# Optimization experiments

Measured on AMD Instinct MI355X. Metric: run time of the kernel, lower is better.

The kernel has to match this reference:

```python
import jax, jax.numpy as jnp
import numpy as np

D_MODEL = 1024
NUM_HEADS = 16
HEAD_DIM = D_MODEL // NUM_HEADS


def setup_inputs() -> dict:
    key = jax.random.key(0)
    k_x, k_wq, k_wo = jax.random.split(key, 3)
    x = jax.random.normal(k_x, (2, 2048, D_MODEL), dtype=jnp.float32)
    # Xavier-uniform init to mirror _reset_parameters
    lim_qkv = float(np.sqrt(6.0 / (D_MODEL + 3 * D_MODEL)))
    lim_o = float(np.sqrt(6.0 / (D_MODEL + D_MODEL)))
    w_qkv = jax.random.uniform(k_wq, (3 * D_MODEL, D_MODEL), jnp.float32, -lim_qkv, lim_qkv)
    b_qkv = jnp.zeros((3 * D_MODEL,), jnp.float32)
    w_o = jax.random.uniform(k_wo, (D_MODEL, D_MODEL), jnp.float32, -lim_o, lim_o)
    b_o = jnp.zeros((D_MODEL,), jnp.float32)
    return {"x": x, "w_qkv": w_qkv, "b_qkv": b_qkv, "w_o": w_o, "b_o": b_o}


def reference(x, w_qkv, b_qkv, w_o, b_o):
    B, T, C = x.shape
    H, Dh = NUM_HEADS, HEAD_DIM
    # Fused QKV projection: [B,T,3C]
    qkv = jnp.einsum('btc,oc->bto', x, w_qkv) + b_qkv
    qkv = qkv.reshape(B, T, 3, H, Dh)
    q = qkv[:, :, 0].transpose(0, 2, 1, 3)  # [B,H,T,Dh]
    k = qkv[:, :, 1].transpose(0, 2, 1, 3)
    v = qkv[:, :, 2].transpose(0, 2, 1, 3)
    scale = 1.0 / jnp.sqrt(jnp.asarray(Dh, x.dtype))
    scores = jnp.einsum('bhqd,bhkd->bhqk', q, k) * scale  # [B,H,T,T]
    attn = jax.nn.softmax(scores, axis=-1)
    out = jnp.einsum('bhqk,bhkd->bhqd', attn, v)  # [B,H,T,Dh]
    out = out.transpose(0, 2, 1, 3).reshape(B, T, C)
    return jnp.einsum('btc,oc->bto', out, w_o) + b_o
```

## Files before the change

### kernel.cpp

```cpp
#include <hip/hip_runtime.h>
#include <math.h>

#define SEQ   2048
#define BATCH 2
#define CDIM  1024
#define NH    16
#define DH    64
#define BH    (BATCH*NH)
#define KVB   64
#define QBLK  128

#define QSCALE 0.18033688011112042f
#define SMSHIFT 12.0f

typedef __attribute__((ext_vector_type(8))) short bf16x8;
typedef __attribute__((ext_vector_type(4))) short s16x4;
typedef __attribute__((ext_vector_type(4))) float f32x4;
typedef __attribute__((ext_vector_type(2))) unsigned u32x2;

__device__ __forceinline__ short f2bf(float f) {
  union { float f; unsigned u; } v; v.f = f;
  unsigned r = (v.u + 0x7FFFu + ((v.u >> 16) & 1u)) >> 16;
  return (short)r;
}
__device__ __forceinline__ float bf2f(short s) {
  union { unsigned u; float f; } v; v.u = ((unsigned)(unsigned short)s) << 16;
  return v.f;
}
__device__ __forceinline__ float fexp2(float x) {
  float r; asm("v_exp_f32 %0, %1" : "=v"(r) : "v"(x)); return r;
}
__device__ __forceinline__ unsigned cvtpk_bf16(float a, float b) {
  unsigned r; asm("v_cvt_pk_bf16_f32 %0, %1, %2" : "=v"(r) : "v"(a), "v"(b));
  return r;
}
__device__ __forceinline__ void gload_lds16(const void* g, void* l) {
  __builtin_amdgcn_global_load_lds(
      (const __attribute__((address_space(1))) void*)g,
      (__attribute__((address_space(3))) void*)l, 16, 0, 0);
}

template<int R>
__device__ __forceinline__ void stage_tile(const short* __restrict__ g,
                                           short* __restrict__ lds, int tid) {
#pragma unroll
  for (int rd = 0; rd < R / 64; ++rd) {
    const int idx = rd * 256 + tid;
    const int row = idx >> 2, ch = idx & 3;
    const int sch = ch ^ ((row >> 1) & 3);
    gload_lds16(&g[(long)row * CDIM + sch * 8], &lds[idx * 8]);
  }
}
__device__ __forceinline__ bf16x8 frag(const short* __restrict__ lds,
                                       int row, int g) {
  const int sch = g ^ ((row >> 1) & 3);
  return *(const bf16x8*)&lds[row * 32 + sch * 8];
}

__device__ __forceinline__ int aswz(int row, int ch) {
  return (row << 6) + ((ch ^ (row & 7)) << 3);
}

__global__ __launch_bounds__(256)
void cvt_hilo2(const float* __restrict__ a, short* __restrict__ ah,
               short* __restrict__ al, int na4,
               const float* __restrict__ b, short* __restrict__ bh,
               short* __restrict__ bl, int nb4) {
  int i = blockIdx.x * 256 + threadIdx.x;
  const float* src; short *dh, *dl;
  if (i < na4) { src = a; dh = ah; dl = al; }
  else { i -= na4; if (i >= nb4) return; src = b; dh = bh; dl = bl; }
  const float4 v = reinterpret_cast<const float4*>(src)[i];
  s16x4 h, l;
  h[0] = f2bf(v.x); h[1] = f2bf(v.y); h[2] = f2bf(v.z); h[3] = f2bf(v.w);
  l[0] = f2bf(v.x - bf2f(h[0]));
  l[1] = f2bf(v.y - bf2f(h[1]));
  l[2] = f2bf(v.z - bf2f(h[2]));
  l[3] = f2bf(v.w - bf2f(h[3]));
  reinterpret_cast<s16x4*>(dh)[i] = h;
  reinterpret_cast<s16x4*>(dl)[i] = l;
}

__global__ __launch_bounds__(256)
void cvt_hilo(const float* __restrict__ in, short* __restrict__ hi,
              short* __restrict__ lo, int n4) {
  const int i = blockIdx.x * 256 + threadIdx.x;
  if (i >= n4) return;
  const float4 v = reinterpret_cast<const float4*>(in)[i];
  s16x4 h, l;
  h[0] = f2bf(v.x); h[1] = f2bf(v.y); h[2] = f2bf(v.z); h[3] = f2bf(v.w);
  l[0] = f2bf(v.x - bf2f(h[0]));
  l[1] = f2bf(v.y - bf2f(h[1]));
  l[2] = f2bf(v.z - bf2f(h[2]));
  l[3] = f2bf(v.w - bf2f(h[3]));
  reinterpret_cast<s16x4*>(hi)[i] = h;
  reinterpret_cast<s16x4*>(lo)[i] = l;
}

__global__ __launch_bounds__(256)
void qkv_mfma(const short* __restrict__ xh, const short* __restrict__ xl,
              const short* __restrict__ wh, const short* __restrict__ wl,
              const float* __restrict__ bias,
              short* __restrict__ qh, short* __restrict__ ql,
              short* __restrict__ kh, short* __restrict__ kl,
              short* __restrict__ vt) {
  __shared__ short S[2][4][128 * 32];
  const int tid  = threadIdx.x;
  const int wave = tid >> 6, lane = tid & 63;
  const int l15  = lane & 15, g = lane >> 4;
  const int wr   = wave >> 1, wc = wave & 1;
  const int wgid = blockIdx.x;
  const int xcd  = wgid & 7, pos = wgid >> 3;
  const int m0   = (xcd * 4 + pos / 24) * 128;
  const int n0   = (pos % 24) * 128;

  const short* Abh = xh + (long)m0 * CDIM;
  const short* Abl = xl + (long)m0 * CDIM;
  const short* Bbh = wh + (long)n0 * CDIM;
  const short* Bbl = wl + (long)n0 * CDIM;

  f32x4 acc[4][4];
#pragma unroll
  for (int mi = 0; mi < 4; ++mi)
#pragma unroll
    for (int ni = 0; ni < 4; ++ni) {
      acc[mi][ni][0] = 0.f; acc[mi][ni][1] = 0.f;
      acc[mi][ni][2] = 0.f; acc[mi][ni][3] = 0.f;
    }

  stage_tile<128>(Abh, S[0][0], tid);
  stage_tile<128>(Abl, S[0][1], tid);
  stage_tile<128>(Bbh, S[0][2], tid);
  stage_tile<128>(Bbl, S[0][3], tid);

  for (int k = 0; k < CDIM / 32; ++k) {
    const int cur = k & 1;
    if (k < CDIM / 32 - 1) {
      const int k1 = (k + 1) * 32;
      stage_tile<128>(Abh + k1, S[cur ^ 1][0], tid);
      stage_tile<128>(Abl + k1, S[cur ^ 1][1], tid);
      stage_tile<128>(Bbh + k1, S[cur ^ 1][2], tid);
      stage_tile<128>(Bbl + k1, S[cur ^ 1][3], tid);
      asm volatile("s_waitcnt vmcnt(8)" ::: "memory");
    } else {
      asm volatile("s_waitcnt vmcnt(0)" ::: "memory");
    }
    __builtin_amdgcn_sched_barrier(0);
    __builtin_amdgcn_s_barrier();
    __builtin_amdgcn_sched_barrier(0);

    bf16x8 ah[4], al2[4], bh2[4], bl2[4];
#pragma unroll
    for (int mi = 0; mi < 4; ++mi) {
      const int r = wr * 64 + mi * 16 + l15;
      ah[mi]  = frag(S[cur][0], r, g);
      al2[mi] = frag(S[cur][1], r, g);
    }
#pragma unroll
    for (int ni = 0; ni < 4; ++ni) {
      const int r = wc * 64 + ni * 16 + l15;
      bh2[ni] = frag(S[cur][2], r, g);
      bl2[ni] = frag(S[cur][3], r, g);
    }
    __builtin_amdgcn_s_setprio(1);
#pragma unroll
    for (int mi = 0; mi < 4; ++mi)
#pragma unroll
      for (int ni = 0; ni < 4; ++ni) {
        acc[mi][ni] = __builtin_amdgcn_mfma_f32_16x16x32_bf16(
            ah[mi], bh2[ni], acc[mi][ni], 0, 0, 0);
        acc[mi][ni] = __builtin_amdgcn_mfma_f32_16x16x32_bf16(
            al2[mi], bh2[ni], acc[mi][ni], 0, 0, 0);
        acc[mi][ni] = __builtin_amdgcn_mfma_f32_16x16x32_bf16(
            ah[mi], bl2[ni], acc[mi][ni], 0, 0, 0);
      }
    __builtin_amdgcn_s_setprio(0);

    __builtin_amdgcn_sched_barrier(0);
    __builtin_amdgcn_s_barrier();
    __builtin_amdgcn_sched_barrier(0);
  }

  const int s = n0 >> 10;
  const int hbase = (n0 & 1023) >> 6;
  if (s < 2) {
    short* hb = (s == 0) ? qh : kh;
    short* lb = (s == 0) ? ql : kl;
    const float sc = (s == 0) ? QSCALE : 1.0f;
    float bv[4];
#pragma unroll
    for (int ni = 0; ni < 4; ++ni) bv[ni] = bias[n0 + wc * 64 + ni * 16 + l15];
    short* T = &S[0][0][0];
#pragma unroll
    for (int p = 0; p < 2; ++p) {
#pragma unroll
      for (int mi = 0; mi < 4; ++mi)
#pragma unroll
        for (int ni = 0; ni < 4; ++ni)
#pragma unroll
          for (int r = 0; r < 4; ++r) {
            const int row = wr * 64 + mi * 16 + g * 4 + r;
            const int col = wc * 64 + ni * 16 + l15;
            const float v = (acc[mi][ni][r] + bv[ni]) * sc;
            const short hv = f2bf(v);
            T[row * 136 + col] = (p == 0) ? hv : f2bf(v - bf2f(hv));
          }
      __syncthreads();
      short* dst = (p == 0) ? hb : lb;
#pragma unroll
      for (int it = 0; it < 8; ++it) {
        const int idx = it * 256 + tid;
        const int row = idx >> 4, c16 = idx & 15;
        const bf16x8 vv = *(const bf16x8*)&T[row * 136 + c16 * 8];
        const int h = hbase + (c16 >> 3), dh0 = (c16 & 7) * 8;
        const int t = m0 + row, bi = t >> 11, tt = t & 2047;
        *(bf16x8*)&dst[(((long)(bi * NH + h)) * SEQ + tt) * DH + dh0] = vv;
      }
      __syncthreads();
    }
  } else {
#pragma unroll
    for (int ni = 0; ni < 4; ++ni) {
      const int n_g = n0 + wc * 64 + ni * 16 + l15;
      const int o = n_g & 1023, h = o >> 6, dh = o & 63;
      const float bvv = bias[n_g];
#pragma unroll
      for (int mi = 0; mi < 4; ++mi) {
        const int mr = m0 + wr * 64 + mi * 16 + g * 4;
        const int bi = mr >> 11, t = mr & 2047;
        s16x4 pv;
#pragma unroll
        for (int r = 0; r < 4; ++r) pv[r] = f2bf(acc[mi][ni][r] + bvv);
        *(s16x4*)&vt[(((long)(bi * NH + h)) * DH + dh) * SEQ + t] = pv;
      }
    }
  }
}

__global__ __launch_bounds__(256)
void fattn_mfma(const short* __restrict__ qhg, const short* __restrict__ qlg,
                const short* __restrict__ khg, const short* __restrict__ klg,
                const short* __restrict__ vtg,
                short* __restrict__ abh, short* __restrict__ abl) {
  __shared__ short Khs[2][KVB * 64];
  __shared__ short Kls[2][KVB * 64];
  __shared__ short Vts[2][DH * 64];
  __shared__ short Ps[QBLK * 64];

  const int tid  = threadIdx.x;
  const int wave = tid >> 6;
  const int lane = tid & 63;
  const int l15  = lane & 15;
  const int g    = lane >> 4;
  const int wgid = blockIdx.x;
  const int xcd  = wgid & 7, pos = wgid >> 3;
  const int bh   = xcd * 4 + (pos >> 4);
  const int q0   = (pos & 15) * QBLK;
  const int qw   = q0 + wave * 32;

  bf16x8 Qh[2][2], Ql[2][2];
#pragma unroll
  for (int qt = 0; qt < 2; ++qt) {
    const long qrow = ((long)bh * SEQ + qw + qt * 16 + l15) * DH;
#pragma unroll
    for (int c = 0; c < 2; ++c) {
      Qh[qt][c] = *(const bf16x8*)&qhg[qrow + c * 32 + g * 8];
      Ql[qt][c] = *(const bf16x8*)&qlg[qrow + c * 32 + g * 8];
    }
  }

  f32x4 o[2][4];
#pragma unroll
  for (int qt = 0; qt < 2; ++qt)
#pragma unroll
    for (int d = 0; d < 4; ++d) {
      o[qt][d][0] = 0.f; o[qt][d][1] = 0.f;
      o[qt][d][2] = 0.f; o[qt][d][3] = 0.f;
    }
  float lrun[2] = {0.f, 0.f};

  long ksrc[2], vsrc[2];
  int ldst[2];
#pragma unroll
  for (int it = 0; it < 2; ++it) {
    const int idx = it * 256 + tid;
    const int srow = idx >> 3;
    const int gch = (idx & 7) ^ (srow & 7);
    ksrc[it] = (long)bh * SEQ * DH + (long)srow * DH + gch * 8;
    vsrc[it] = ((long)bh * DH + srow) * SEQ + gch * 8;
    ldst[it] = idx * 8;
  }

#pragma unroll
  for (int it = 0; it < 2; ++it) {
    gload_lds16(&khg[ksrc[it]], &Khs[0][ldst[it]]);
    gload_lds16(&klg[ksrc[it]], &Kls[0][ldst[it]]);
    gload_lds16(&vtg[vsrc[it]], &Vts[0][ldst[it]]);
  }
  __syncthreads();

  int cur = 0;
  for (int kt = 0; kt < SEQ / KVB; ++kt) {
    if (kt + 1 < SEQ / KVB) {
#pragma unroll
      for (int it = 0; it < 2; ++it) {
        const long ko = ksrc[it] + (long)(kt + 1) * (KVB * DH);
        gload_lds16(&khg[ko], &Khs[cur ^ 1][ldst[it]]);
        gload_lds16(&klg[ko], &Kls[cur ^ 1][ldst[it]]);
        gload_lds16(&vtg[vsrc[it] + (kt + 1) * KVB], &Vts[cur ^ 1][ldst[it]]);
      }
    }

    const short* Kc = Khs[cur];
    const short* Lc = Kls[cur];
    f32x4 s[2][4];
    __builtin_amdgcn_s_setprio(1);
#pragma unroll
    for (int kc = 0; kc < 4; ++kc) {
      const int a0 = aswz(kc * 16 + l15, g);
      const int a1 = aswz(kc * 16 + l15, 4 + g);
      const bf16x8 kb0 = *(const bf16x8*)&Kc[a0];
      const bf16x8 lb0 = *(const bf16x8*)&Lc[a0];
      const bf16x8 kb1 = *(const bf16x8*)&Kc[a1];
      const bf16x8 lb1 = *(const bf16x8*)&Lc[a1];
#pragma unroll
      for (int qt = 0; qt < 2; ++qt) {
        f32x4 a; a[0] = 0.f; a[1] = 0.f; a[2] = 0.f; a[3] = 0.f;
        a = __builtin_amdgcn_mfma_f32_16x16x32_bf16(kb0, Qh[qt][0], a, 0, 0, 0);
        a = __builtin_amdgcn_mfma_f32_16x16x32_bf16(kb0, Ql[qt][0], a, 0, 0, 0);
        a = __builtin_amdgcn_mfma_f32_16x16x32_bf16(lb0, Qh[qt][0], a, 0, 0, 0);
        a = __builtin_amdgcn_mfma_f32_16x16x32_bf16(kb1, Qh[qt][1], a, 0, 0, 0);
        a = __builtin_amdgcn_mfma_f32_16x16x32_bf16(kb1, Ql[qt][1], a, 0, 0, 0);
        a = __builtin_amdgcn_mfma_f32_16x16x32_bf16(lb1, Qh[qt][1], a, 0, 0, 0);
        s[qt][kc] = a;
      }
    }
    __builtin_amdgcn_s_setprio(0);

#pragma unroll
    for (int qt = 0; qt < 2; ++qt) {
      const int row = wave * 32 + qt * 16 + l15;
#pragma unroll
      for (int kc = 0; kc < 4; ++kc) {
        const float p0 = fexp2(s[qt][kc][0] - SMSHIFT);
        const float p1 = fexp2(s[qt][kc][1] - SMSHIFT);
        const float p2 = fexp2(s[qt][kc][2] - SMSHIFT);
        const float p3 = fexp2(s[qt][kc][3] - SMSHIFT);
        lrun[qt] += (p0 + p1) + (p2 + p3);
        u32x2 w; w[0] = cvtpk_bf16(p0, p1); w[1] = cvtpk_bf16(p2, p3);
        const int ch = (2 * kc + (g >> 1)) ^ (row & 7);
        *(u32x2*)&Ps[(row << 6) + ch * 8 + (g & 1) * 4] = w;
      }
    }

    const short* Vc = Vts[cur];
    __builtin_amdgcn_s_setprio(1);
#pragma unroll
    for (int kk = 0; kk < 2; ++kk) {
      bf16x8 vf[4];
#pragma unroll
      for (int d = 0; d < 4; ++d)
        vf[d] = *(const bf16x8*)&Vc[aswz(d * 16 + l15, kk * 4 + g)];
#pragma unroll
      for (int qt = 0; qt < 2; ++qt) {
        const bf16x8 pa =
            *(const bf16x8*)&Ps[aswz(wave * 32 + qt * 16 + l15, kk * 4 + g)];
#pragma unroll
        for (int d = 0; d < 4; ++d)
          o[qt][d] = __builtin_amdgcn_mfma_f32_16x16x32_bf16(
              pa, vf[d], o[qt][d], 0, 0, 0);
      }
    }
    __builtin_amdgcn_s_setprio(0);

    __syncthreads();
    cur ^= 1;
  }

  const int b = bh >> 4, hh = bh & 15;
#pragma unroll
  for (int qt = 0; qt < 2; ++qt) {
    float rs = lrun[qt];
    rs += __shfl_xor(rs, 16);
    rs += __shfl_xor(rs, 32);
#pragma unroll
    for (int r = 0; r < 4; ++r) {
      const float lv = __shfl(rs, 16 * g + 4 * g + r);
      const float inv = 1.0f / lv;
      const int t = qw + qt * 16 + 4 * g + r;
      const long base = ((long)(b * SEQ + t)) * CDIM + hh * DH + l15;
#pragma unroll
      for (int d = 0; d < 4; ++d) {
        const float v = o[qt][d][r] * inv;
        const short hv = f2bf(v);
        abh[base + d * 16] = hv;
        abl[base + d * 16] = f2bf(v - bf2f(hv));
      }
    }
  }
}

__global__ __launch_bounds__(256)
void out_mfma(const short* __restrict__ ah, const short* __restrict__ al,
              const short* __restrict__ wh, const short* __restrict__ wl,
              const float* __restrict__ bias, float* __restrict__ out) {
  __shared__ short S[2][12288];
  const int tid  = threadIdx.x;
  const int wave = tid >> 6, lane = tid & 63;
  const int l15  = lane & 15, g = lane >> 4;
  const int wr   = wave >> 1, wc = wave & 1;
  const int m0   = blockIdx.y * 128, n0 = blockIdx.x * 64;

  const short* Abh = ah + (long)m0 * CDIM;
  const short* Abl = al + (long)m0 * CDIM;
  const short* Bbh = wh + (long)n0 * CDIM;
  const short* Bbl = wl + (long)n0 * CDIM;

  f32x4 acc[4][2];
#pragma unroll
  for (int mi = 0; mi < 4; ++mi)
#pragma unroll
    for (int ni = 0; ni < 2; ++ni) {
      acc[mi][ni][0] = 0.f; acc[mi][ni][1] = 0.f;
      acc[mi][ni][2] = 0.f; acc[mi][ni][3] = 0.f;
    }

  stage_tile<128>(Abh, &S[0][0], tid);
  stage_tile<128>(Abl, &S[0][4096], tid);
  stage_tile<64>(Bbh, &S[0][8192], tid);
  stage_tile<64>(Bbl, &S[0][10240], tid);
  __syncthreads();

  for (int k = 0; k < CDIM / 32; ++k) {
    const int cur = k & 1;
    if (k < CDIM / 32 - 1) {
      const int k1 = (k + 1) * 32;
      stage_tile<128>(Abh + k1, &S[cur ^ 1][0], tid);
      stage_tile<128>(Abl + k1, &S[cur ^ 1][4096], tid);
      stage_tile<64>(Bbh + k1, &S[cur ^ 1][8192], tid);
      stage_tile<64>(Bbl + k1, &S[cur ^ 1][10240], tid);
    }
    bf16x8 af[4], af2[4], bf1[2], bf2[2];
#pragma unroll
    for (int mi = 0; mi < 4; ++mi) {
      const int r = wr * 64 + mi * 16 + l15;
      af[mi]  = frag(&S[cur][0], r, g);
      af2[mi] = frag(&S[cur][4096], r, g);
    }
#pragma unroll
    for (int ni = 0; ni < 2; ++ni) {
      const int r = wc * 32 + ni * 16 + l15;
      bf1[ni] = frag(&S[cur][8192], r, g);
      bf2[ni] = frag(&S[cur][10240], r, g);
    }
#pragma unroll
    for (int mi = 0; mi < 4; ++mi)
#pragma unroll
      for (int ni = 0; ni < 2; ++ni) {
        acc[mi][ni] = __builtin_amdgcn_mfma_f32_16x16x32_bf16(
            af[mi], bf1[ni], acc[mi][ni], 0, 0, 0);
        acc[mi][ni] = __builtin_amdgcn_mfma_f32_16x16x32_bf16(
            af2[mi], bf1[ni], acc[mi][ni], 0, 0, 0);
        acc[mi][ni] = __builtin_amdgcn_mfma_f32_16x16x32_bf16(
            af[mi], bf2[ni], acc[mi][ni], 0, 0, 0);
      }
    __syncthreads();
  }

#pragma unroll
  for (int ni = 0; ni < 2; ++ni) {
    const int n = n0 + wc * 32 + ni * 16 + l15;
    const float bv = bias[n];
#pragma unroll
    for (int mi = 0; mi < 4; ++mi) {
#pragma unroll
      for (int r = 0; r < 4; ++r) {
        const int m = m0 + wr * 64 + mi * 16 + g * 4 + r;
        out[(long)m * CDIM + n] = acc[mi][ni][r] + bv;
      }
    }
  }
}

__global__ __launch_bounds__(256)
void qkv_gemm_f32(const float* __restrict__ x, const float* __restrict__ w,
                  const float* __restrict__ bias,
                  short* __restrict__ qh, short* __restrict__ ql,
                  short* __restrict__ kh, short* __restrict__ kl,
                  short* __restrict__ vt) {
  __shared__ float As[16][65];
  __shared__ float Bs[16][65];
  const int tid = threadIdx.x;
  const int tx = tid & 15, ty = tid >> 4;
  const int m0 = blockIdx.y * 64;
  const int n0 = blockIdx.x * 64;
  const int lr = tid >> 2;
  const int lc = (tid & 3) << 2;
  float acc[4][4] = {};
  const float* ap = x + (long)(m0 + lr) * CDIM + lc;
  const float* bp = w + (long)(n0 + lr) * CDIM + lc;
  for (int k0 = 0; k0 < CDIM; k0 += 16) {
    float4 av = *reinterpret_cast<const float4*>(ap + k0);
    float4 bv = *reinterpret_cast<const float4*>(bp + k0);
    __syncthreads();
    As[lc + 0][lr] = av.x; As[lc + 1][lr] = av.y;
    As[lc + 2][lr] = av.z; As[lc + 3][lr] = av.w;
    Bs[lc + 0][lr] = bv.x; Bs[lc + 1][lr] = bv.y;
    Bs[lc + 2][lr] = bv.z; Bs[lc + 3][lr] = bv.w;
    __syncthreads();
#pragma unroll
    for (int kk = 0; kk < 16; ++kk) {
      float a[4], bb[4];
#pragma unroll
      for (int i = 0; i < 4; ++i) a[i] = As[kk][ty * 4 + i];
#pragma unroll
      for (int j = 0; j < 4; ++j) bb[j] = Bs[kk][tx * 4 + j];
#pragma unroll
      for (int i = 0; i < 4; ++i)
#pragma unroll
        for (int j = 0; j < 4; ++j)
          acc[i][j] = fmaf(a[i], bb[j], acc[i][j]);
    }
  }
  const int s = n0 >> 10;
  const int hh = (n0 & 1023) >> 6;
  const float4 bq = *reinterpret_cast<const float4*>(&bias[n0 + tx * 4]);
  if (s < 2) {
    const float scale = (s == 0) ? QSCALE : 1.0f;
    short* hb = (s == 0) ? qh : kh;
    short* lb = (s == 0) ? ql : kl;
#pragma unroll
    for (int i = 0; i < 4; ++i) {
      const int m = m0 + ty * 4 + i;
      const int bi = m >> 11, t = m & 2047;
      float v0 = (acc[i][0] + bq.x) * scale;
      float v1 = (acc[i][1] + bq.y) * scale;
      float v2 = (acc[i][2] + bq.z) * scale;
      float v3 = (acc[i][3] + bq.w) * scale;
      s16x4 hv, lv;
      hv[0] = f2bf(v0); hv[1] = f2bf(v1); hv[2] = f2bf(v2); hv[3] = f2bf(v3);
      lv[0] = f2bf(v0 - bf2f(hv[0]));
      lv[1] = f2bf(v1 - bf2f(hv[1]));
      lv[2] = f2bf(v2 - bf2f(hv[2]));
      lv[3] = f2bf(v3 - bf2f(hv[3]));
      const long base = (((long)(bi * NH + hh)) * SEQ + t) * DH + tx * 4;
      *(s16x4*)&hb[base] = hv;
      *(s16x4*)&lb[base] = lv;
    }
  } else {
#pragma unroll
    for (int i = 0; i < 4; ++i) {
      const int m = m0 + ty * 4 + i;
      const int bi = m >> 11, t = m & 2047;
      float vv[4] = {acc[i][0] + bq.x, acc[i][1] + bq.y,
                     acc[i][2] + bq.z, acc[i][3] + bq.w};
#pragma unroll
      for (int j = 0; j < 4; ++j)
        vt[((long)(bi * NH + hh) * DH + tx * 4 + j) * SEQ + t] = f2bf(vv[j]);
    }
  }
}

__global__ __launch_bounds__(256)
void out_gemm_f32(const short* __restrict__ ah, const short* __restrict__ al,
                  const float* __restrict__ w,
                  const float* __restrict__ bias, float* __restrict__ out) {
  __shared__ float As[16][65];
  __shared__ float Bs[16][65];
  const int tid = threadIdx.x;
  const int tx = tid & 15, ty = tid >> 4;
  const int m0 = blockIdx.y * 64;
  const int n0 = blockIdx.x * 64;
  const int lr = tid >> 2;
  const int lc = (tid & 3) << 2;
  float acc[4][4] = {};
  const long arow = (long)(m0 + lr) * CDIM + lc;
  const float* bp = w + (long)(n0 + lr) * CDIM + lc;
  for (int k0 = 0; k0 < CDIM; k0 += 16) {
    s16x4 hv = *(const s16x4*)&ah[arow + k0];
    s16x4 lv = *(const s16x4*)&al[arow + k0];
    float4 bv = *reinterpret_cast<const float4*>(bp + k0);
    __syncthreads();
#pragma unroll
    for (int j = 0; j < 4; ++j) As[lc + j][lr] = bf2f(hv[j]) + bf2f(lv[j]);
    Bs[lc + 0][lr] = bv.x; Bs[lc + 1][lr] = bv.y;
    Bs[lc + 2][lr] = bv.z; Bs[lc + 3][lr] = bv.w;
    __syncthreads();
#pragma unroll
    for (int kk = 0; kk < 16; ++kk) {
      float av2[4], bb[4];
#pragma unroll
      for (int i = 0; i < 4; ++i) av2[i] = As[kk][ty * 4 + i];
#pragma unroll
      for (int j = 0; j < 4; ++j) bb[j] = Bs[kk][tx * 4 + j];
#pragma unroll
      for (int i = 0; i < 4; ++i)
#pragma unroll
        for (int j = 0; j < 4; ++j)
          acc[i][j] = fmaf(av2[i], bb[j], acc[i][j]);
    }
  }
  const float4 bq = *reinterpret_cast<const float4*>(&bias[n0 + tx * 4]);
#pragma unroll
  for (int i = 0; i < 4; ++i) {
    const int m = m0 + ty * 4 + i;
    float4 v;
    v.x = acc[i][0] + bq.x; v.y = acc[i][1] + bq.y;
    v.z = acc[i][2] + bq.z; v.w = acc[i][3] + bq.w;
    *reinterpret_cast<float4*>(&out[(long)m * CDIM + n0 + tx * 4]) = v;
  }
}

extern "C" void kernel_launch(void* const* d_in, const int* in_sizes, int n_in,
                              void* d_out, int out_size, void* d_ws, size_t ws_size,
                              hipStream_t stream) {
  (void)in_sizes; (void)n_in; (void)out_size;
  const float* x     = (const float*)d_in[0];
  const float* w_qkv = (const float*)d_in[1];
  const float* b_qkv = (const float*)d_in[2];
  const float* w_o   = (const float*)d_in[3];
  const float* b_o   = (const float*)d_in[4];
  float* out = (float*)d_out;

  const size_t NEED = 71303168;
  if (ws_size >= NEED) {
    short* base = (short*)d_ws;
    short* xh  = base;
    short* xl  = base + 4194304;
    short* wqh = base + 8388608;
    short* wql = base + 11534336;
    short* qh  = base + 14680064;
    short* ql  = base + 18874368;
    short* kh  = base + 23068672;
    short* kl  = base + 27262976;
    short* vt  = base + 31457280;
    short* woh = wqh;
    short* wol = wqh + 1048576;
    short* abh = xh;
    short* abl = xl;

    cvt_hilo2<<<7168, 256, 0, stream>>>(x, xh, xl, 1048576,
                                        w_qkv, wqh, wql, 786432);
    qkv_mfma<<<768, 256, 0, stream>>>(xh, xl, wqh, wql, b_qkv,
                                      qh, ql, kh, kl, vt);
    cvt_hilo<<<1024, 256, 0, stream>>>(w_o, woh, wol, 262144);
    fattn_mfma<<<512, 256, 0, stream>>>(qh, ql, kh, kl, vt, abh, abl);
    out_mfma<<<dim3(16, 32), 256, 0, stream>>>(abh, abl, woh, wol, b_o, out);
  } else {
    short* qh  = (short*)d_ws;
    short* ql  = qh + 4194304;
    short* kh  = ql + 4194304;
    short* kl  = kh + 4194304;
    short* vt  = kl + 4194304;
    short* abh = vt + 4194304;
    short* abl = abh + 4194304;

    qkv_gemm_f32<<<dim3(48, 64), 256, 0, stream>>>(x, w_qkv, b_qkv,
                                                   qh, ql, kh, kl, vt);
    fattn_mfma<<<512, 256, 0, stream>>>(qh, ql, kh, kl, vt, abh, abl);
    out_gemm_f32<<<dim3(16, 64), 256, 0, stream>>>(abh, abl, w_o, b_o, out);
  }
}
```

Measured before the change: 207.2 us.

## Restructure QKV GEMM into 4-stage single-barrier pipeline over split-bf16 passes

The QKV projection kernel now treats the three hi/lo bf16 product terms (xh*wh, xl*wh, xh*wl) as 96 sequential K-steps, each staging only one A tile and one B tile. These tiles go into a 4-slot LDS ring with a prefetch distance of two, which allows one barrier per iteration instead of two. It also halves the fragment registers and LDS per stage, and adds an occupancy hint of 4 blocks per CU. In exchange there are three times as many loop iterations and barriers, each with less MFMA work to hide load latency. Accumulation order across the hi/lo terms also changes.

```diff
diff --git a/kernel.cpp b/kernel.cpp
--- a/kernel.cpp
+++ b/kernel.cpp
@@ -97,14 +97,14 @@
   reinterpret_cast<s16x4*>(lo)[i] = l;
 }
 
-__global__ __launch_bounds__(256)
+__global__ __launch_bounds__(256, 4)
 void qkv_mfma(const short* __restrict__ xh, const short* __restrict__ xl,
               const short* __restrict__ wh, const short* __restrict__ wl,
               const float* __restrict__ bias,
               short* __restrict__ qh, short* __restrict__ ql,
               short* __restrict__ kh, short* __restrict__ kl,
               short* __restrict__ vt) {
-  __shared__ short S[2][4][128 * 32];
+  __shared__ short L[32768];
   const int tid  = threadIdx.x;
   const int wave = tid >> 6, lane = tid & 63;
   const int l15  = lane & 15, g = lane >> 4;
@@ -114,10 +114,8 @@
   const int m0   = (xcd * 4 + pos / 24) * 128;
   const int n0   = (pos % 24) * 128;
 
-  const short* Abh = xh + (long)m0 * CDIM;
-  const short* Abl = xl + (long)m0 * CDIM;
-  const short* Bbh = wh + (long)n0 * CDIM;
-  const short* Bbl = wl + (long)n0 * CDIM;
+  const long abase = (long)m0 * CDIM;
+  const long bbase = (long)n0 * CDIM;
 
   f32x4 acc[4][4];
 #pragma unroll
@@ -128,20 +126,24 @@
       acc[mi][ni][2] = 0.f; acc[mi][ni][3] = 0.f;
     }
 
-  stage_tile<128>(Abh, S[0][0], tid);
-  stage_tile<128>(Abl, S[0][1], tid);
-  stage_tile<128>(Bbh, S[0][2], tid);
-  stage_tile<128>(Bbl, S[0][3], tid);
-
-  for (int k = 0; k < CDIM / 32; ++k) {
-    const int cur = k & 1;
-    if (k < CDIM / 32 - 1) {
-      const int k1 = (k + 1) * 32;
-      stage_tile<128>(Abh + k1, S[cur ^ 1][0], tid);
-      stage_tile<128>(Abl + k1, S[cur ^ 1][1], tid);
-      stage_tile<128>(Bbh + k1, S[cur ^ 1][2], tid);
-      stage_tile<128>(Bbl + k1, S[cur ^ 1][3], tid);
+#define QA(ks) ((((ks) >> 5) == 1 ? xl : xh) + abase + (((ks) & 31) * 32))
+#define QB(ks) ((((ks) >> 5) == 2 ? wl : wh) + bbase + (((ks) & 31) * 32))
+
+  stage_tile<128>(QA(0), &L[0 * 8192], tid);
+  stage_tile<128>(QB(0), &L[0 * 8192 + 4096], tid);
+  stage_tile<128>(QA(1), &L[1 * 8192], tid);
+  stage_tile<128>(QB(1), &L[1 * 8192 + 4096], tid);
+
+#pragma unroll 4
+  for (int k = 0; k < 96; ++k) {
+    const int p = k & 3;
+    if (k < 94) {
+      const int pn = (k + 2) & 3;
+      stage_tile<128>(QA(k + 2), &L[pn * 8192], tid);
+      stage_tile<128>(QB(k + 2), &L[pn * 8192 + 4096], tid);
       asm volatile("s_waitcnt vmcnt(8)" ::: "memory");
+    } else if (k == 94) {
+      asm volatile("s_waitcnt vmcnt(4)" ::: "memory");
     } else {
       asm volatile("s_waitcnt vmcnt(0)" ::: "memory");
     }
@@ -149,37 +151,27 @@
     __builtin_amdgcn_s_barrier();
     __builtin_amdgcn_sched_barrier(0);
 
-    bf16x8 ah[4], al2[4], bh2[4], bl2[4];
-#pragma unroll
-    for (int mi = 0; mi < 4; ++mi) {
-      const int r = wr * 64 + mi * 16 + l15;
-      ah[mi]  = frag(S[cur][0], r, g);
-      al2[mi] = frag(S[cur][1], r, g);
-    }
-#pragma unroll
-    for (int ni = 0; ni < 4; ++ni) {
-      const int r = wc * 64 + ni * 16 + l15;
-      bh2[ni] = frag(S[cur][2], r, g);
-      bl2[ni] = frag(S[cur][3], r, g);
-    }
+    const short* As = &L[p * 8192];
+    const short* Bs = &L[p * 8192 + 4096];
+    bf16x8 af[4], bf[4];
+#pragma unroll
+    for (int mi = 0; mi < 4; ++mi) af[mi] = frag(As, wr * 64 + mi * 16 + l15, g);
+#pragma unroll
+    for (int ni = 0; ni < 4; ++ni) bf[ni] = frag(Bs, wc * 64 + ni * 16 + l15, g);
+
     __builtin_amdgcn_s_setprio(1);
 #pragma unroll
     for (int mi = 0; mi < 4; ++mi)
 #pragma unroll
-      for (int ni = 0; ni < 4; ++ni) {
+      for (int ni = 0; ni < 4; ++ni)
         acc[mi][ni] = __builtin_amdgcn_mfma_f32_16x16x32_bf16(
-            ah[mi], bh2[ni], acc[mi][ni], 0, 0, 0);
-        acc[mi][ni] = __builtin_amdgcn_mfma_f32_16x16x32_bf16(
-            al2[mi], bh2[ni], acc[mi][ni], 0, 0, 0);
-        acc[mi][ni] = __builtin_amdgcn_mfma_f32_16x16x32_bf16(
-            ah[mi], bl2[ni], acc[mi][ni], 0, 0, 0);
-      }
+            af[mi], bf[ni], acc[mi][ni], 0, 0, 0);
     __builtin_amdgcn_s_setprio(0);
-
-    __builtin_amdgcn_sched_barrier(0);
-    __builtin_amdgcn_s_barrier();
-    __builtin_amdgcn_sched_barrier(0);
-  }
+  }
+#undef QA
+#undef QB
+
+  __syncthreads();
 
   const int s = n0 >> 10;
   const int hbase = (n0 & 1023) >> 6;
@@ -190,7 +182,7 @@
     float bv[4];
 #pragma unroll
     for (int ni = 0; ni < 4; ++ni) bv[ni] = bias[n0 + wc * 64 + ni * 16 + l15];
-    short* T = &S[0][0][0];
+    short* T = L;
 #pragma unroll
     for (int p = 0; p < 2; ++p) {
 #pragma unroll
```

Result: slower. 229.6 us (+10.8%).
